# Kernel optimization log

Hardware: AMD Instinct MI355X
Metric: run time of the kernel (lower is better)

The kernel has to match this reference:

```python
import jax, jax.numpy as jnp
import numpy as np

D_MODEL, D_INNER, D_STATE, D_CONV, DT_RANK = 4, 8, 16, 4, 1


def _build_perms(N, H, W):
    # center-out 2D spatial order
    yy, xx = np.meshgrid(np.arange(H), np.arange(W), indexing='ij')
    cy, cx = H // 2, W // 2
    d2 = (yy - cy) ** 2 + (xx - cx) ** 2
    sp = np.argsort(d2.reshape(-1), kind='stable')          # (H*W,)
    HW = H * W
    # scanA: for each frame t, full center-out spatial sweep
    scanA = (np.arange(N)[:, None] * HW + sp[None, :]).reshape(-1)
    # scanB: for each spatial pos (in center-out order), zig-zag over frames
    fwd = np.arange(N)
    bwd = fwd[::-1]
    tids = np.where((np.arange(HW) % 2 == 0)[:, None], fwd[None, :], bwd[None, :])  # (HW, N)
    scanB = (tids * HW + sp[:, None]).reshape(-1)
    perms = np.stack([scanA, scanB, scanA[::-1], scanB[::-1]], axis=0)  # (4, L)
    return jnp.asarray(perms)


def _dwconv1d(x_bcl, w, b, pad, groups):
    # x: (B, C, L), w: (C, 1, K) depthwise
    y = jax.lax.conv_general_dilated(x_bcl, w, (1,), [pad],
                                     feature_group_count=groups,
                                     dimension_numbers=('NCH', 'OIH', 'NCH'))
    return y + b[None, :, None]


def _forward(x, dwconv_w, dwconv_b, in_proj_w, conv1d_w, conv1d_b,
             x_proj_w, dt_proj_w, dt_proj_b, A_log, Dp, out_proj_w, ln_g, ln_b):
    B, N, H, W = x.shape
    L = N * H * W
    perms = _build_perms(N, H, W)                 # (4, L) int, static
    xf = x.reshape(B, L)
    seqs = xf[:, perms]                            # (B, 4, L) gather along 4 scans
    seqs = _dwconv1d(seqs, dwconv_w, dwconv_b, (1, 1), 4)
    u = jax.nn.silu(seqs.transpose(0, 2, 1))       # (B, L, 4)
    # ---- Mamba(d_model=4) ----
    xz = jnp.einsum('bld,ed->ble', u, in_proj_w)   # (B, L, 2*d_inner)
    xm, z = xz[..., :D_INNER], xz[..., D_INNER:]
    xc = _dwconv1d(xm.transpose(0, 2, 1), conv1d_w, conv1d_b, (D_CONV - 1, 0), D_INNER)
    xm = jax.nn.silu(xc.transpose(0, 2, 1))        # (B, L, 8) causal conv + SiLU
    x_dbl = jnp.einsum('bld,ed->ble', xm, x_proj_w)  # (B, L, dt_rank+2*d_state)
    dt = x_dbl[..., :DT_RANK]
    Bm = x_dbl[..., DT_RANK:DT_RANK + D_STATE]     # (B, L, 16)
    Cm = x_dbl[..., DT_RANK + D_STATE:]            # (B, L, 16)
    dt = jax.nn.softplus(jnp.einsum('blr,dr->bld', dt, dt_proj_w) + dt_proj_b)  # (B, L, 8)
    A = -jnp.exp(A_log)                            # (8, 16)
    dA = jnp.exp(dt[..., None] * A)                # (B, L, 8, 16)
    dBx = dt[..., None] * Bm[:, :, None, :] * xm[..., None]  # (B, L, 8, 16)

    def step(h, inp):
        dA_t, dBx_t, C_t = inp
        h = dA_t * h + dBx_t                       # (B, 8, 16)
        return h, jnp.einsum('bds,bs->bd', h, C_t)

    h0 = jnp.zeros((B, D_INNER, D_STATE), x.dtype)
    _, ys = jax.lax.scan(step, h0, (dA.transpose(1, 0, 2, 3),
                                    dBx.transpose(1, 0, 2, 3),
                                    Cm.transpose(1, 0, 2)))
    y = ys.transpose(1, 0, 2) + xm * Dp            # (B, L, 8)
    y = y * jax.nn.silu(z)
    out = jnp.einsum('bld,ed->ble', y, out_proj_w)  # (B, L, 4)
    # ---- LayerNorm(4) ----
    mu = out.mean(-1, keepdims=True)
    var = ((out - mu) ** 2).mean(-1, keepdims=True)
    out = (out - mu) * jax.lax.rsqrt(var + 1e-5) * ln_g + ln_b
    # rec[:, inv[i]] = out[:, :, i]  <=>  rec_i = out[:, perms[i], i]
    rec = jnp.take_along_axis(out, perms.T[None], axis=1)  # (B, L, 4)
    return rec.mean(-1).reshape(B, N, H, W)


def setup_inputs() -> dict:
    key = jax.random.key(0)
    ks = jax.random.split(key, 12)
    s = 0.1
    x = jax.random.normal(ks[0], (4, 6, 128, 128), jnp.float32)
    return {
        'x': x,
        'dwconv_w': jax.random.normal(ks[1], (4, 1, 3), jnp.float32) * s,
        'dwconv_b': jnp.zeros((4,), jnp.float32),
        'in_proj_w': jax.random.normal(ks[2], (2 * D_INNER, D_MODEL), jnp.float32) * s,
        'conv1d_w': jax.random.normal(ks[3], (D_INNER, 1, D_CONV), jnp.float32) * s,
        'conv1d_b': jnp.zeros((D_INNER,), jnp.float32),
        'x_proj_w': jax.random.normal(ks[4], (DT_RANK + 2 * D_STATE, D_INNER), jnp.float32) * s,
        'dt_proj_w': jax.random.normal(ks[5], (D_INNER, DT_RANK), jnp.float32) * s,
        'dt_proj_b': jnp.full((D_INNER,), -2.0, jnp.float32),
        'A_log': jnp.log(jnp.tile(jnp.arange(1, D_STATE + 1, dtype=jnp.float32), (D_INNER, 1))),
        'Dp': jnp.ones((D_INNER,), jnp.float32),
        'out_proj_w': jax.random.normal(ks[6], (D_MODEL, D_INNER), jnp.float32) * s,
        'ln_g': jnp.ones((4,), jnp.float32),
        'ln_b': jnp.zeros((4,), jnp.float32),
    }


def reference(x, dwconv_w, dwconv_b, in_proj_w, conv1d_w, conv1d_b,
              x_proj_w, dt_proj_w, dt_proj_b, A_log, Dp, out_proj_w, ln_g, ln_b):
    return _forward(x, dwconv_w, dwconv_b, in_proj_w, conv1d_w, conv1d_b,
                    x_proj_w, dt_proj_w, dt_proj_b, A_log, Dp, out_proj_w, ln_g, ln_b)
```

## Files before the change

kernel.cpp:

```cpp
#include <hip/hip_runtime.h>
#include <math.h>

#define HWSZ  16384
#define LTOT  98304
#define NB    4
#define TCH   96
#define NCH   1024
#define GCH   64
#define NGRP  16
#define SD    100
#define NBL (NB * LTOT)

__device__ __forceinline__ float siluf(float x){
  return x * __builtin_amdgcn_rcpf(1.f + __expf(-x));
}
__device__ __forceinline__ float softplusf(float x){
  return fmaxf(x, 0.f) + __logf(1.f + __expf(-fabsf(x)));
}

__device__ __forceinline__ float red16(float x){
  int v;
  v = __float_as_int(x);
  x += __int_as_float(__builtin_amdgcn_update_dpp(0, v, 0xB1, 0xF, 0xF, true));
  v = __float_as_int(x);
  x += __int_as_float(__builtin_amdgcn_update_dpp(0, v, 0x4E, 0xF, 0xF, true));
  v = __float_as_int(x);
  x += __int_as_float(__builtin_amdgcn_update_dpp(0, v, 0x141, 0xF, 0xF, true));
  v = __float_as_int(x);
  x += __int_as_float(__builtin_amdgcn_update_dpp(0, v, 0x140, 0xF, 0xF, true));
  return x;
}

__device__ __forceinline__ int rho0(int i, const int* __restrict__ sp){
  int n = i >> 14; int r = i & (HWSZ - 1);
  return (n << 14) + sp[r];
}
__device__ __forceinline__ int rho1(int i, const int* __restrict__ sp){
  unsigned ui = (unsigned)i;
  unsigned r = ui / 6u; unsigned n = ui - r * 6u;
  unsigned t = (r & 1u) ? (5u - n) : n;
  return (int)((t << 14) + (unsigned)sp[r]);
}

__global__ __launch_bounds__(256) void k_rank(int* __restrict__ sp){
  __shared__ int hist[8193];
  __shared__ int part[256];
  const int tid = threadIdx.x;
  for (int v = tid; v < 8193; v += 256) hist[v] = 0;
  __syncthreads();
  for (int jj = tid; jj < HWSZ; jj += 256){
    int dy = (jj >> 7) - 64, dx = (jj & 127) - 64;
    atomicAdd(&hist[dy*dy + dx*dx], 1);
  }
  __syncthreads();
  const int base = tid * 33;
  {
    int sum = 0;
    for (int m = 0; m < 33; ++m){ int v = base + m; if (v < 8193) sum += hist[v]; }
    part[tid] = sum;
  }
  __syncthreads();
  if (tid == 0){
    int run = 0;
    for (int t = 0; t < 256; ++t){ int c = part[t]; part[t] = run; run += c; }
  }
  __syncthreads();
  {
    int run = part[tid];
    for (int m = 0; m < 33; ++m){
      int v = base + m;
      if (v < 8193){ int c = hist[v]; hist[v] = run; run += c; }
    }
  }
  __syncthreads();

  const int j = blockIdx.x * 256 + tid;
  const int y = j >> 7, x = j & 127;
  const int dy = y - 64, dx = x - 64;
  const int v = dy*dy + dx*dx;
  int cnt = hist[v];
  const int r = __float2int_rd(sqrtf((float)v));
  int yp0 = 64 - r; if (yp0 < 0) yp0 = 0;
  int yp1 = 64 + r + 1; if (yp1 > y) yp1 = y;
  for (int yp = yp0; yp < yp1; ++yp){
    int dyp = yp - 64;
    int tt = v - dyp*dyp;
    int rr = __float2int_rn(sqrtf((float)tt));
    if (rr * rr == tt){
      cnt += (rr <= 64) ? 1 : 0;
      cnt += (rr >= 1 && rr <= 63) ? 1 : 0;
    }
  }
  if (x > 64) cnt += 1;
  sp[cnt] = j;
}

__global__ __launch_bounds__(128, 4)
void k_scan(const float* __restrict__ X,
            const float* __restrict__ dww, const float* __restrict__ dwb,
            const float* __restrict__ ipw,
            const float* __restrict__ c1w, const float* __restrict__ c1b,
            const float* __restrict__ xpw,
            const float* __restrict__ dtpw, const float* __restrict__ dtpb,
            const float* __restrict__ Alog,
            const int* __restrict__ sp,
            float* __restrict__ chA, float* __restrict__ chB,
            float* __restrict__ y0g, float* __restrict__ sgg,
            float* __restrict__ xmg, float* __restrict__ zgg,
            float* __restrict__ Cgg)
{
  const int c = blockIdx.x, b = blockIdx.y;
  const int c0 = c * TCH;
  const int tid = threadIdx.x;
  const float* Xb = X + (size_t)b * LTOT;

  __shared__ __align__(16) float s_pre[(TCH + 3) * 9];
  __shared__ __align__(16) float s_dt[8 * SD];
  __shared__ __align__(16) float s_dxm[8 * SD];
  __shared__ __align__(16) float s_Bv[16 * SD];
  __shared__ __align__(16) float s_Cv[16 * SD];

  if (tid < TCH + 3){
    const int m = tid;
    const int i = c0 - 3 + m;
    if (i < 0){
      #pragma unroll
      for (int d = 0; d < 8; ++d) s_pre[m*9 + d] = 0.f;
    } else {
      const int i2 = LTOT - 1 - i;
      const bool okm = (i > 0), okp = (i < LTOT - 1);
      int q[12];
      q[0]  = okm ? rho0(i - 1, sp) : 0;
      q[1]  =       rho0(i,     sp);
      q[2]  = okp ? rho0(i + 1, sp) : 0;
      q[3]  = okm ? rho1(i - 1, sp) : 0;
      q[4]  =       rho1(i,     sp);
      q[5]  = okp ? rho1(i + 1, sp) : 0;
      q[6]  = okm ? rho0(i2 + 1, sp) : 0;
      q[7]  =       rho0(i2,     sp);
      q[8]  = okp ? rho0(i2 - 1, sp) : 0;
      q[9]  = okm ? rho1(i2 + 1, sp) : 0;
      q[10] =       rho1(i2,     sp);
      q[11] = okp ? rho1(i2 - 1, sp) : 0;
      float xv[12];
      #pragma unroll
      for (int t = 0; t < 12; ++t) xv[t] = Xb[q[t]];
      if (!okm){ xv[0] = 0.f; xv[3] = 0.f; xv[6] = 0.f; xv[9]  = 0.f; }
      if (!okp){ xv[2] = 0.f; xv[5] = 0.f; xv[8] = 0.f; xv[11] = 0.f; }
      float u[4];
      #pragma unroll
      for (int k = 0; k < 4; ++k){
        float acc = dwb[k];
        acc = fmaf(dww[k*3+0], xv[k*3+0], acc);
        acc = fmaf(dww[k*3+1], xv[k*3+1], acc);
        acc = fmaf(dww[k*3+2], xv[k*3+2], acc);
        u[k] = siluf(acc);
      }
      #pragma unroll
      for (int d = 0; d < 8; ++d){
        float acc =      ipw[d*4+0] * u[0];
        acc = fmaf(ipw[d*4+1], u[1], acc);
        acc = fmaf(ipw[d*4+2], u[2], acc);
        acc = fmaf(ipw[d*4+3], u[3], acc);
        s_pre[m*9 + d] = acc;
      }
      if (m >= 3){
        float zz[8];
        #pragma unroll
        for (int d = 0; d < 8; ++d){
          float acc =      ipw[(8+d)*4+0] * u[0];
          acc = fmaf(ipw[(8+d)*4+1], u[1], acc);
          acc = fmaf(ipw[(8+d)*4+2], u[2], acc);
          acc = fmaf(ipw[(8+d)*4+3], u[3], acc);
          zz[d] = siluf(acc);
        }
        const size_t ib8 = ((size_t)b * LTOT + i) * 8;
        *reinterpret_cast<float4*>(zgg + ib8)     = make_float4(zz[0], zz[1], zz[2], zz[3]);
        *reinterpret_cast<float4*>(zgg + ib8 + 4) = make_float4(zz[4], zz[5], zz[6], zz[7]);
      }
    }
  }
  __syncthreads();

  if (tid < TCH){
    const int t = tid;
    float xm[8];
    #pragma unroll
    for (int d = 0; d < 8; ++d){
      float acc = c1b[d];
      #pragma unroll
      for (int tau = 0; tau < 4; ++tau)
        acc = fmaf(c1w[d*4+tau], s_pre[(t+tau)*9 + d], acc);
      xm[d] = siluf(acc);
    }
    const size_t ib8 = ((size_t)b * LTOT + c0 + t) * 8;
    *reinterpret_cast<float4*>(xmg + ib8)     = make_float4(xm[0], xm[1], xm[2], xm[3]);
    *reinterpret_cast<float4*>(xmg + ib8 + 4) = make_float4(xm[4], xm[5], xm[6], xm[7]);
    float dtr = xpw[0] * xm[0];
    #pragma unroll
    for (int d = 1; d < 8; ++d) dtr = fmaf(xpw[d], xm[d], dtr);
    float Cl[16];
    #pragma unroll
    for (int s = 0; s < 16; ++s){
      float acc = xpw[(1+s)*8] * xm[0];
      #pragma unroll
      for (int d = 1; d < 8; ++d) acc = fmaf(xpw[(1+s)*8+d], xm[d], acc);
      s_Bv[s*SD + t] = acc;
      float acc2 = xpw[(17+s)*8] * xm[0];
      #pragma unroll
      for (int d = 1; d < 8; ++d) acc2 = fmaf(xpw[(17+s)*8+d], xm[d], acc2);
      s_Cv[s*SD + t] = acc2;
      Cl[s] = acc2;
    }
    float* pcg = Cgg + ((size_t)b * LTOT + c0 + t) * 16;
    *reinterpret_cast<float4*>(pcg)      = make_float4(Cl[0],  Cl[1],  Cl[2],  Cl[3]);
    *reinterpret_cast<float4*>(pcg + 4)  = make_float4(Cl[4],  Cl[5],  Cl[6],  Cl[7]);
    *reinterpret_cast<float4*>(pcg + 8)  = make_float4(Cl[8],  Cl[9],  Cl[10], Cl[11]);
    *reinterpret_cast<float4*>(pcg + 12) = make_float4(Cl[12], Cl[13], Cl[14], Cl[15]);
    #pragma unroll
    for (int d = 0; d < 8; ++d){
      float dtv = softplusf(fmaf(dtpw[d], dtr, dtpb[d]));
      s_dt[d*SD + t]  = dtv;
      s_dxm[d*SD + t] = dtv * xm[d];
    }
  }
  __syncthreads();

  {
    const int d = tid >> 4, s = tid & 15;
    const float Ads = -__expf(Alog[tid]);
    float h = 0.f, run = 0.f;
    const float* pdt = s_dt + d*SD;
    const float* pdx = s_dxm + d*SD;
    const float* pB  = s_Bv + s*SD;
    const float* pC  = s_Cv + s*SD;
    float* yb = y0g + ((size_t)b * NCH + c) * 768 + d * 96;
    float* sb = sgg + ((size_t)b * NCH + c) * 768 + d * 96;
    for (int t0 = 0; t0 < TCH; t0 += 4){
      const float4 dt4 = *reinterpret_cast<const float4*>(pdt + t0);
      const float4 dx4 = *reinterpret_cast<const float4*>(pdx + t0);
      const float4 B4  = *reinterpret_cast<const float4*>(pB + t0);
      const float4 C4  = *reinterpret_cast<const float4*>(pC + t0);
      const float r0 = run + dt4.x, r1 = r0 + dt4.y, r2 = r1 + dt4.z, r3 = r2 + dt4.w;
      run = r3;
      float y0, y1, y2, y3;
      { float dA = __expf(dt4.x*Ads); h = fmaf(dA, h, dx4.x*B4.x); y0 = h*C4.x; }
      { float dA = __expf(dt4.y*Ads); h = fmaf(dA, h, dx4.y*B4.y); y1 = h*C4.y; }
      { float dA = __expf(dt4.z*Ads); h = fmaf(dA, h, dx4.z*B4.z); y2 = h*C4.z; }
      { float dA = __expf(dt4.w*Ads); h = fmaf(dA, h, dx4.w*B4.w); y3 = h*C4.w; }
      y0 = red16(y0); y1 = red16(y1); y2 = red16(y2); y3 = red16(y3);
      if (s == 0)
        *reinterpret_cast<float4*>(yb + t0) = make_float4(y0, y1, y2, y3);
      else if (s == 1)
        *reinterpret_cast<float4*>(sb + t0) = make_float4(r0, r1, r2, r3);
    }
    const size_t base = ((size_t)b * NCH + c) * 128 + tid;
    chA[base] = __expf(Ads * run);
    chB[base] = h;
  }
}

__global__ __launch_bounds__(128) void k_comb1(const float* __restrict__ chA,
                                               const float* __restrict__ chB,
                                               float* __restrict__ hpre,
                                               float* __restrict__ apre,
                                               float* __restrict__ GA,
                                               float* __restrict__ GB){
  const int j = blockIdx.x;
  const int g = j >> 2, b = j & 3;
  const int idx = threadIdx.x;
  const size_t base = ((size_t)b * NCH + (size_t)g * GCH) * 128 + idx;
  float h = 0.f, a = 1.f;
  float A_[8], B_[8];
  #pragma unroll
  for (int m = 0; m < 8; ++m){ A_[m] = chA[base + (size_t)m*128]; B_[m] = chB[base + (size_t)m*128]; }
  for (int cc = 0; cc < GCH; cc += 8){
    float A2[8], B2[8];
    if (cc + 8 < GCH){
      #pragma unroll
      for (int m = 0; m < 8; ++m){ A2[m] = chA[base + (size_t)(cc+8+m)*128]; B2[m] = chB[base + (size_t)(cc+8+m)*128]; }
    } else {
      #pragma unroll
      for (int m = 0; m < 8; ++m){ A2[m] = 0.f; B2[m] = 0.f; }
    }
    #pragma unroll
    for (int m = 0; m < 8; ++m){
      hpre[base + (size_t)(cc+m)*128] = h;
      apre[base + (size_t)(cc+m)*128] = a;
      h = fmaf(A_[m], h, B_[m]);
      a *= A_[m];
    }
    #pragma unroll
    for (int m = 0; m < 8; ++m){ A_[m] = A2[m]; B_[m] = B2[m]; }
  }
  GA[(size_t)(g*4+b)*128 + idx] = a;
  GB[(size_t)(g*4+b)*128 + idx] = h;
}

__global__ __launch_bounds__(128, 4)
void k_corr(const float* __restrict__ Cgg,
            const float* __restrict__ xmg, const float* __restrict__ zgg,
            const float* __restrict__ sgg, const float* __restrict__ y0g,
            const float* __restrict__ Alog, const float* __restrict__ Dp,
            const float* __restrict__ opw,
            const float* __restrict__ lng, const float* __restrict__ lnb,
            const float* __restrict__ hpre, const float* __restrict__ apre,
            const float* __restrict__ GA, const float* __restrict__ GB,
            float* __restrict__ outbuf)
{
  const int c = blockIdx.x, b = blockIdx.y;
  const int c0 = c * TCH;
  const int tid = threadIdx.x;
  const size_t cb = (size_t)b * NCH + c;

  __shared__ float s_hA[256];
  __shared__ __align__(16) float s_yf[768];

  {
    const int g = c >> 6;
    const float hp = hpre[cb * 128 + tid];
    const float ap = apre[cb * 128 + tid];
    float Hv = 0.f;
    for (int gp = 0; gp < g; ++gp){
      const float ga = GA[(size_t)gp*512 + (size_t)b*128 + tid];
      const float gb = GB[(size_t)gp*512 + (size_t)b*128 + tid];
      Hv = fmaf(ga, Hv, gb);
    }
    s_hA[tid]       = fmaf(ap, Hv, hp);
    s_hA[128 + tid] = -__expf(Alog[tid]);
  }
  __syncthreads();

  {
    const int d = tid >> 4, tsub = tid & 15;
    float w[16], A16[16];
    #pragma unroll
    for (int s = 0; s < 16; ++s){
      w[s]   = s_hA[d*16 + s];
      A16[s] = s_hA[128 + d*16 + s];
    }
    const float* psg = sgg + cb * 768 + d * 96;
    const float* py0 = y0g + cb * 768 + d * 96;
    const float* pC0 = Cgg + ((size_t)b * LTOT + c0) * 16;
    for (int t = tsub; t < TCH; t += 16){
      const float sg = psg[t];
      float acc = py0[t];
      const float* pc = pC0 + t*16;
      #pragma unroll
      for (int s4 = 0; s4 < 16; s4 += 4){
        const float4 C4 = *reinterpret_cast<const float4*>(pc + s4);
        acc = fmaf(C4.x, __expf(A16[s4+0]*sg) * w[s4+0], acc);
        acc = fmaf(C4.y, __expf(A16[s4+1]*sg) * w[s4+1], acc);
        acc = fmaf(C4.z, __expf(A16[s4+2]*sg) * w[s4+2], acc);
        acc = fmaf(C4.w, __expf(A16[s4+3]*sg) * w[s4+3], acc);
      }
      s_yf[d*96 + t] = acc;
    }
  }
  __syncthreads();

  if (tid < TCH){
    const int t = tid;
    const int i = c0 + t;
    const size_t ib8 = ((size_t)b * LTOT + i) * 8;
    const float4 x0 = *reinterpret_cast<const float4*>(xmg + ib8);
    const float4 x1 = *reinterpret_cast<const float4*>(xmg + ib8 + 4);
    const float4 z0 = *reinterpret_cast<const float4*>(zgg + ib8);
    const float4 z1 = *reinterpret_cast<const float4*>(zgg + ib8 + 4);
    float y[8];
    y[0] = fmaf(x0.x, Dp[0], s_yf[0*96 + t]) * z0.x;
    y[1] = fmaf(x0.y, Dp[1], s_yf[1*96 + t]) * z0.y;
    y[2] = fmaf(x0.z, Dp[2], s_yf[2*96 + t]) * z0.z;
    y[3] = fmaf(x0.w, Dp[3], s_yf[3*96 + t]) * z0.w;
    y[4] = fmaf(x1.x, Dp[4], s_yf[4*96 + t]) * z1.x;
    y[5] = fmaf(x1.y, Dp[5], s_yf[5*96 + t]) * z1.y;
    y[6] = fmaf(x1.z, Dp[6], s_yf[6*96 + t]) * z1.z;
    y[7] = fmaf(x1.w, Dp[7], s_yf[7*96 + t]) * z1.w;
    float o[4];
    #pragma unroll
    for (int e = 0; e < 4; ++e){
      float acc = opw[e*8] * y[0];
      #pragma unroll
      for (int d = 1; d < 8; ++d) acc = fmaf(opw[e*8+d], y[d], acc);
      o[e] = acc;
    }
    const float mu = 0.25f * (o[0] + o[1] + o[2] + o[3]);
    const float v0 = o[0] - mu, v1 = o[1] - mu, v2 = o[2] - mu, v3 = o[3] - mu;
    const float inv = rsqrtf(0.25f * (v0*v0 + v1*v1 + v2*v2 + v3*v3) + 1e-5f);
    const size_t base = (size_t)b * LTOT + i;
    outbuf[0*NBL + base] = fmaf(v0 * inv, lng[0], lnb[0]);
    outbuf[1*NBL + base] = fmaf(v1 * inv, lng[1], lnb[1]);
    outbuf[2*NBL + base] = fmaf(v2 * inv, lng[2], lnb[2]);
    outbuf[3*NBL + base] = fmaf(v3 * inv, lng[3], lnb[3]);
  }
}

__global__ __launch_bounds__(256) void k_final(const float* __restrict__ outbuf,
                                               const int* __restrict__ sp,
                                               float* __restrict__ out){
  const int l = blockIdx.x * 256 + threadIdx.x;
  const int b = blockIdx.y;
  const int q0 = rho0(l, sp), q1 = rho1(l, sp);
  const int j  = LTOT - 1 - l;
  const int q2 = rho0(j, sp), q3 = rho1(j, sp);
  const size_t pb = (size_t)b * LTOT;
  out[pb + l] = 0.25f * (outbuf[0*NBL + pb + q0] + outbuf[1*NBL + pb + q1] +
                         outbuf[2*NBL + pb + q2] + outbuf[3*NBL + pb + q3]);
}

extern "C" void kernel_launch(void* const* d_in, const int* in_sizes, int n_in,
                              void* d_out, int out_size, void* d_ws, size_t ws_size,
                              hipStream_t stream) {
  const float* X    = (const float*)d_in[0];
  const float* dww  = (const float*)d_in[1];
  const float* dwb  = (const float*)d_in[2];
  const float* ipw  = (const float*)d_in[3];
  const float* c1w  = (const float*)d_in[4];
  const float* c1b  = (const float*)d_in[5];
  const float* xpw  = (const float*)d_in[6];
  const float* dtpw = (const float*)d_in[7];
  const float* dtpb = (const float*)d_in[8];
  const float* Alog = (const float*)d_in[9];
  const float* Dp   = (const float*)d_in[10];
  const float* opw  = (const float*)d_in[11];
  const float* lng  = (const float*)d_in[12];
  const float* lnb  = (const float*)d_in[13];
  float* out = (float*)d_out;

  int* wsI    = (int*)d_ws;
  int* sp     = wsI;
  float* chA  = (float*)(wsI + 16384);
  float* chB  = chA  + 524288;
  float* hpre = chB  + 524288;
  float* apre = hpre + 524288;
  float* GA   = apre + 524288;
  float* GB   = GA + 8192;
  float* y0g  = GB + 8192;
  float* sgg  = y0g + 3145728;
  float* xmg  = sgg + 3145728;
  float* zgg  = xmg + 3145728;
  float* Cgg  = zgg + 3145728;
  float* outbuf = Cgg + 6291456;

  k_rank<<<64, 256, 0, stream>>>(sp);
  k_scan<<<dim3(NCH, NB), 128, 0, stream>>>(X, dww, dwb, ipw, c1w, c1b, xpw,
      dtpw, dtpb, Alog, sp, chA, chB, y0g, sgg, xmg, zgg, Cgg);
  k_comb1<<<64, 128, 0, stream>>>(chA, chB, hpre, apre, GA, GB);
  k_corr<<<dim3(NCH, NB), 128, 0, stream>>>(Cgg, xmg, zgg, sgg, y0g,
      Alog, Dp, opw, lng, lnb, hpre, apre, GA, GB, outbuf);
  k_final<<<dim3(LTOT / 256, NB), 256, 0, stream>>>(outbuf, sp, out);
}
```

Before: 182.9 us.

## Recompute C projection in correction kernel and transpose-reduce scan outputs

The scan kernel no longer writes the 16-wide C projection to global memory. The correction kernel instead recomputes it from the stored xm values into shared memory, which removes a large global write and read pair in exchange for extra FMAs. Separately, the per-timestep 16-lane DPP reduction is replaced by a transposed butterfly reduction over 16 timesteps. In that scheme each lane ends up holding one timestep's sum, which cuts the number of DPP ops and lets all lanes store y values.

```diff
diff --git a/kernel.cpp b/kernel.cpp
--- a/kernel.cpp
+++ b/kernel.cpp
@@ -18,17 +18,9 @@
   return fmaxf(x, 0.f) + __logf(1.f + __expf(-fabsf(x)));
 }
 
-__device__ __forceinline__ float red16(float x){
-  int v;
-  v = __float_as_int(x);
-  x += __int_as_float(__builtin_amdgcn_update_dpp(0, v, 0xB1, 0xF, 0xF, true));
-  v = __float_as_int(x);
-  x += __int_as_float(__builtin_amdgcn_update_dpp(0, v, 0x4E, 0xF, 0xF, true));
-  v = __float_as_int(x);
-  x += __int_as_float(__builtin_amdgcn_update_dpp(0, v, 0x141, 0xF, 0xF, true));
-  v = __float_as_int(x);
-  x += __int_as_float(__builtin_amdgcn_update_dpp(0, v, 0x140, 0xF, 0xF, true));
-  return x;
+template<int CTRL>
+__device__ __forceinline__ float dppadd(float x){
+  return x + __int_as_float(__builtin_amdgcn_update_dpp(0, __float_as_int(x), CTRL, 0xF, 0xF, true));
 }
 
 __device__ __forceinline__ int rho0(int i, const int* __restrict__ sp){
@@ -106,8 +98,7 @@
             const int* __restrict__ sp,
             float* __restrict__ chA, float* __restrict__ chB,
             float* __restrict__ y0g, float* __restrict__ sgg,
-            float* __restrict__ xmg, float* __restrict__ zgg,
-            float* __restrict__ Cgg)
+            float* __restrict__ xmg, float* __restrict__ zgg)
 {
   const int c = blockIdx.x, b = blockIdx.y;
   const int c0 = c * TCH;
@@ -199,7 +190,6 @@
     float dtr = xpw[0] * xm[0];
     #pragma unroll
     for (int d = 1; d < 8; ++d) dtr = fmaf(xpw[d], xm[d], dtr);
-    float Cl[16];
     #pragma unroll
     for (int s = 0; s < 16; ++s){
       float acc = xpw[(1+s)*8] * xm[0];
@@ -210,13 +200,7 @@
       #pragma unroll
       for (int d = 1; d < 8; ++d) acc2 = fmaf(xpw[(17+s)*8+d], xm[d], acc2);
       s_Cv[s*SD + t] = acc2;
-      Cl[s] = acc2;
-    }
-    float* pcg = Cgg + ((size_t)b * LTOT + c0 + t) * 16;
-    *reinterpret_cast<float4*>(pcg)      = make_float4(Cl[0],  Cl[1],  Cl[2],  Cl[3]);
-    *reinterpret_cast<float4*>(pcg + 4)  = make_float4(Cl[4],  Cl[5],  Cl[6],  Cl[7]);
-    *reinterpret_cast<float4*>(pcg + 8)  = make_float4(Cl[8],  Cl[9],  Cl[10], Cl[11]);
-    *reinterpret_cast<float4*>(pcg + 12) = make_float4(Cl[12], Cl[13], Cl[14], Cl[15]);
+    }
     #pragma unroll
     for (int d = 0; d < 8; ++d){
       float dtv = softplusf(fmaf(dtpw[d], dtr, dtpb[d]));
@@ -228,6 +212,7 @@
 
   {
     const int d = tid >> 4, s = tid & 15;
+    const bool b3 = (s & 8) != 0, b2 = (s & 4) != 0, b1 = (s & 2) != 0, b0 = (s & 1) != 0;
     const float Ads = -__expf(Alog[tid]);
     float h = 0.f, run = 0.f;
     const float* pdt = s_dt + d*SD;
@@ -236,23 +221,39 @@
     const float* pC  = s_Cv + s*SD;
     float* yb = y0g + ((size_t)b * NCH + c) * 768 + d * 96;
     float* sb = sgg + ((size_t)b * NCH + c) * 768 + d * 96;
-    for (int t0 = 0; t0 < TCH; t0 += 4){
-      const float4 dt4 = *reinterpret_cast<const float4*>(pdt + t0);
-      const float4 dx4 = *reinterpret_cast<const float4*>(pdx + t0);
-      const float4 B4  = *reinterpret_cast<const float4*>(pB + t0);
-      const float4 C4  = *reinterpret_cast<const float4*>(pC + t0);
-      const float r0 = run + dt4.x, r1 = r0 + dt4.y, r2 = r1 + dt4.z, r3 = r2 + dt4.w;
-      run = r3;
-      float y0, y1, y2, y3;
-      { float dA = __expf(dt4.x*Ads); h = fmaf(dA, h, dx4.x*B4.x); y0 = h*C4.x; }
-      { float dA = __expf(dt4.y*Ads); h = fmaf(dA, h, dx4.y*B4.y); y1 = h*C4.y; }
-      { float dA = __expf(dt4.z*Ads); h = fmaf(dA, h, dx4.z*B4.z); y2 = h*C4.z; }
-      { float dA = __expf(dt4.w*Ads); h = fmaf(dA, h, dx4.w*B4.w); y3 = h*C4.w; }
-      y0 = red16(y0); y1 = red16(y1); y2 = red16(y2); y3 = red16(y3);
-      if (s == 0)
-        *reinterpret_cast<float4*>(yb + t0) = make_float4(y0, y1, y2, y3);
-      else if (s == 1)
-        *reinterpret_cast<float4*>(sb + t0) = make_float4(r0, r1, r2, r3);
+    for (int t0 = 0; t0 < TCH; t0 += 16){
+      float y[16];
+      #pragma unroll
+      for (int tt = 0; tt < 16; tt += 4){
+        const float4 dt4 = *reinterpret_cast<const float4*>(pdt + t0 + tt);
+        const float4 dx4 = *reinterpret_cast<const float4*>(pdx + t0 + tt);
+        const float4 B4  = *reinterpret_cast<const float4*>(pB + t0 + tt);
+        const float4 C4  = *reinterpret_cast<const float4*>(pC + t0 + tt);
+        const float r0 = run + dt4.x, r1 = r0 + dt4.y, r2 = r1 + dt4.z, r3 = r2 + dt4.w;
+        run = r3;
+        { float dA = __expf(dt4.x*Ads); h = fmaf(dA, h, dx4.x*B4.x); y[tt+0] = h*C4.x; }
+        { float dA = __expf(dt4.y*Ads); h = fmaf(dA, h, dx4.y*B4.y); y[tt+1] = h*C4.y; }
+        { float dA = __expf(dt4.z*Ads); h = fmaf(dA, h, dx4.z*B4.z); y[tt+2] = h*C4.z; }
+        { float dA = __expf(dt4.w*Ads); h = fmaf(dA, h, dx4.w*B4.w); y[tt+3] = h*C4.w; }
+        if (s == 1)
+          *reinterpret_cast<float4*>(sb + t0 + tt) = make_float4(r0, r1, r2, r3);
+      }
+      #pragma unroll
+      for (int j = 0; j < 16; ++j) y[j] = dppadd<0x140>(y[j]);
+      if (b3){
+        #pragma unroll
+        for (int j = 0; j < 8; ++j) y[j] = y[j+8];
+      }
+      #pragma unroll
+      for (int j = 0; j < 8; ++j) y[j] = dppadd<0x141>(y[j]);
+      if (b2){ y[0] = y[4]; y[1] = y[5]; y[2] = y[6]; y[3] = y[7]; }
+      #pragma unroll
+      for (int j = 0; j < 4; ++j) y[j] = dppadd<0x4E>(y[j]);
+      if (b1){ y[0] = y[2]; y[1] = y[3]; }
+      y[0] = dppadd<0xB1>(y[0]);
+      y[1] = dppadd<0xB1>(y[1]);
+      if (b0) y[0] = y[1];
+      yb[t0 + s] = y[0];
     }
     const size_t base = ((size_t)b * NCH + c) * 128 + tid;
     chA[base] = __expf(Ads * run);
@@ -298,9 +299,9 @@
 }
 
 __global__ __launch_bounds__(128, 4)
-void k_corr(const float* __restrict__ Cgg,
-            const float* __restrict__ xmg, const float* __restrict__ zgg,
+void k_corr(const float* __restrict__ xmg, const float* __restrict__ zgg,
             const float* __restrict__ sgg, const float* __restrict__ y0g,
+            const float* __restrict__ xpw,
             const float* __restrict__ Alog, const float* __restrict__ Dp,
             const float* __restrict__ opw,
             const float* __restrict__ lng, const float* __restrict__ lnb,
@@ -315,6 +316,7 @@
 
   __shared__ float s_hA[256];
   __shared__ __align__(16) float s_yf[768];
+  __shared__ __align__(16) float s_Ct[96 * 20];
 
   {
     const int g = c >> 6;
@@ -329,6 +331,21 @@
     s_hA[tid]       = fmaf(ap, Hv, hp);
     s_hA[128 + tid] = -__expf(Alog[tid]);
   }
+  if (tid < TCH){
+    const int t = tid;
+    const size_t ib8 = ((size_t)b * LTOT + c0 + t) * 8;
+    const float4 x0 = *reinterpret_cast<const float4*>(xmg + ib8);
+    const float4 x1 = *reinterpret_cast<const float4*>(xmg + ib8 + 4);
+    const float xm[8] = {x0.x, x0.y, x0.z, x0.w, x1.x, x1.y, x1.z, x1.w};
+    float* pct = s_Ct + t*20;
+    #pragma unroll
+    for (int s = 0; s < 16; ++s){
+      float acc = xpw[(17+s)*8] * xm[0];
+      #pragma unroll
+      for (int d = 1; d < 8; ++d) acc = fmaf(xpw[(17+s)*8+d], xm[d], acc);
+      pct[s] = acc;
+    }
+  }
   __syncthreads();
 
   {
@@ -341,11 +358,10 @@
     }
     const float* psg = sgg + cb * 768 + d * 96;
     const float* py0 = y0g + cb * 768 + d * 96;
-    const float* pC0 = Cgg + ((size_t)b * LTOT + c0) * 16;
     for (int t = tsub; t < TCH; t += 16){
       const float sg = psg[t];
       float acc = py0[t];
-      const float* pc = pC0 + t*16;
+      const float* pc = s_Ct + t*20;
       #pragma unroll
       for (int s4 = 0; s4 < 16; s4 += 4){
         const float4 C4 = *reinterpret_cast<const float4*>(pc + s4);
@@ -439,14 +455,13 @@
   float* sgg  = y0g + 3145728;
   float* xmg  = sgg + 3145728;
   float* zgg  = xmg + 3145728;
-  float* Cgg  = zgg + 3145728;
-  float* outbuf = Cgg + 6291456;
+  float* outbuf = zgg + 3145728;
 
   k_rank<<<64, 256, 0, stream>>>(sp);
   k_scan<<<dim3(NCH, NB), 128, 0, stream>>>(X, dww, dwb, ipw, c1w, c1b, xpw,
-      dtpw, dtpb, Alog, sp, chA, chB, y0g, sgg, xmg, zgg, Cgg);
+      dtpw, dtpb, Alog, sp, chA, chB, y0g, sgg, xmg, zgg);
   k_comb1<<<64, 128, 0, stream>>>(chA, chB, hpre, apre, GA, GB);
-  k_corr<<<dim3(NCH, NB), 128, 0, stream>>>(Cgg, xmg, zgg, sgg, y0g,
+  k_corr<<<dim3(NCH, NB), 128, 0, stream>>>(xmg, zgg, sgg, y0g, xpw,
       Alog, Dp, opw, lng, lnb, hpre, apre, GA, GB, outbuf);
   k_final<<<dim3(LTOT / 256, NB), 256, 0, stream>>>(outbuf, sp, out);
 }
```

Measured after the change: 173.7 us. -5.1%, faster.
